# Performance work log

Hardware: AMD Instinct MI355X
Metric: run time of the kernel (lower is better)

The kernel has to match this reference:

```python
import jax, jax.numpy as jnp
import numpy as np

B, C, H, W = 32, 256, 128, 128
VIEWS, K = 9, 3
PAD = (K - 1) // 2


def setup_inputs() -> dict:
    key = jax.random.key(0)
    k1, k2, k3, k4, k5 = jax.random.split(key, 5)
    x = jax.random.normal(k1, (B, C, H, W), dtype=jnp.float32)
    kernels_u = jax.random.normal(k2, (VIEWS, 1, C, K, K), dtype=jnp.float32) * 0.01
    kernels_v = jax.random.normal(k3, (VIEWS, 1, C, K, K), dtype=jnp.float32) * 0.01
    u_indices = jax.random.randint(k4, (B,), 0, VIEWS)
    v_indices = jax.random.randint(k5, (B,), 0, VIEWS)
    return {"x": x, "kernels_u": kernels_u, "kernels_v": kernels_v,
            "u_indices": u_indices, "v_indices": v_indices}


def reference(x, kernels_u, kernels_v, u_indices, v_indices):
    b, c, h, w = x.shape
    # Gather per-sample kernels: [B,1,C,3,3] each
    k_u = kernels_u[u_indices]
    k_v = kernels_v[v_indices]
    # [B,2,C,3,3] -> grouped-conv weights [2B, C, 3, 3]
    weights = jnp.concatenate([k_u, k_v], axis=1).reshape(b * 2, c, K, K)
    # Reflect-pad then treat batch as groups: lhs [1, B*C, H+2p, W+2p]
    x_pad = jnp.pad(x, ((0, 0), (0, 0), (PAD, PAD), (PAD, PAD)), mode="reflect")
    lhs = x_pad.reshape(1, b * c, h + 2 * PAD, w + 2 * PAD)
    out = jax.lax.conv_general_dilated(
        lhs, weights,
        window_strides=(1, 1), padding="VALID",
        dimension_numbers=("NCHW", "OIHW", "NCHW"),
        feature_group_count=b,
    )  # [1, 2B, H, W]
    return out.reshape(b, 2, h, w)
```

## Files before the change

kernel.cpp:

```cpp
#include <hip/hip_runtime.h>

constexpr int Bc = 32;
constexpr int Cc = 256;
constexpr int Hc = 128;
constexpr int Wc = 128;
constexpr int HWc = Hc * Wc;
constexpr int CHUNKS = 4;
constexpr int CPC = Cc / CHUNKS;
constexpr int ROWS = 16;
constexpr int TILES = Hc / ROWS;

__global__ __launch_bounds__(512) void zero_out_kernel(float4* __restrict__ out4) {
    int i = blockIdx.x * 512 + threadIdx.x;
    out4[i] = make_float4(0.f, 0.f, 0.f, 0.f);
}

__global__ __launch_bounds__(512) void modbank_kernel(
    const float* __restrict__ x,
    const float* __restrict__ ku,
    const float* __restrict__ kv,
    const int*   __restrict__ ui,
    const int*   __restrict__ vi,
    float* __restrict__ out)
{
    __shared__ float4 swu[CPC * 3];
    __shared__ float4 swv[CPC * 3];

    const int tile  = blockIdx.x;
    const int b     = blockIdx.y;
    const int chunk = blockIdx.z;
    const int c0    = chunk * CPC;
    const int tid   = threadIdx.x;

    const int uview = ui[b];
    const int vview = vi[b];
    const float* gu = ku + (size_t)uview * (Cc * 9) + c0 * 9;
    const float* gv = kv + (size_t)vview * (Cc * 9) + c0 * 9;
    float* su = (float*)swu;
    float* sv = (float*)swv;
    for (int i = tid; i < CPC * 9; i += 512) {
        int c = i / 9;
        int k = i - c * 9;
        su[c * 12 + k] = gu[i];
        sv[c * 12 + k] = gv[i];
    }
    __syncthreads();

    const int w4 = tid & 31;
    const int r  = tid >> 5;
    const int h  = tile * ROWS + r;
    const int hm = (h == 0)      ? 1      : h - 1;
    const int hp = (h == Hc - 1) ? Hc - 2 : h + 1;

    const float* pm = x + ((size_t)(b * Cc + c0) * Hc + hm) * Wc + w4 * 4;
    const float* p0 = x + ((size_t)(b * Cc + c0) * Hc + h ) * Wc + w4 * 4;
    const float* pp = x + ((size_t)(b * Cc + c0) * Hc + hp) * Wc + w4 * 4;

    float4 au = make_float4(0.f, 0.f, 0.f, 0.f);
    float4 av = make_float4(0.f, 0.f, 0.f, 0.f);

    auto row_acc = [](float l, const float4& v, float rt,
                      float wa, float wb, float wc, float4& acc) {
        acc.x = fmaf(l,   wa, fmaf(v.x, wb, fmaf(v.y, wc, acc.x)));
        acc.y = fmaf(v.x, wa, fmaf(v.y, wb, fmaf(v.z, wc, acc.y)));
        acc.z = fmaf(v.y, wa, fmaf(v.z, wb, fmaf(v.w, wc, acc.z)));
        acc.w = fmaf(v.z, wa, fmaf(v.w, wb, fmaf(rt,  wc, acc.w)));
    };

    for (int ci = 0; ci < CPC; ++ci) {
        const float4 vm = *(const float4*)pm;
        const float4 v0 = *(const float4*)p0;
        const float4 vp = *(const float4*)pp;
        pm += HWc; p0 += HWc; pp += HWc;

        const float4 u0 = swu[ci * 3 + 0];
        const float4 u1 = swu[ci * 3 + 1];
        const float4 u2 = swu[ci * 3 + 2];
        const float4 q0 = swv[ci * 3 + 0];
        const float4 q1 = swv[ci * 3 + 1];
        const float4 q2 = swv[ci * 3 + 2];

        float lm = __shfl_up(vm.w, 1);  float rm = __shfl_down(vm.x, 1);
        float l0 = __shfl_up(v0.w, 1);  float r0 = __shfl_down(v0.x, 1);
        float lp = __shfl_up(vp.w, 1);  float rp = __shfl_down(vp.x, 1);
        if (w4 == 0)  { lm = vm.y; l0 = v0.y; lp = vp.y; }
        if (w4 == 31) { rm = vm.z; r0 = v0.z; rp = vp.z; }

        row_acc(lm, vm, rm, u0.x, u0.y, u0.z, au);
        row_acc(l0, v0, r0, u0.w, u1.x, u1.y, au);
        row_acc(lp, vp, rp, u1.z, u1.w, u2.x, au);
        row_acc(lm, vm, rm, q0.x, q0.y, q0.z, av);
        row_acc(l0, v0, r0, q0.w, q1.x, q1.y, av);
        row_acc(lp, vp, rp, q1.z, q1.w, q2.x, av);
    }

    float* ou = out + ((size_t)(b * 2 + 0) * Hc + h) * Wc + w4 * 4;
    float* ov = out + ((size_t)(b * 2 + 1) * Hc + h) * Wc + w4 * 4;
    atomicAdd(ou + 0, au.x); atomicAdd(ou + 1, au.y);
    atomicAdd(ou + 2, au.z); atomicAdd(ou + 3, au.w);
    atomicAdd(ov + 0, av.x); atomicAdd(ov + 1, av.y);
    atomicAdd(ov + 2, av.z); atomicAdd(ov + 3, av.w);
}

extern "C" void kernel_launch(void* const* d_in, const int* in_sizes, int n_in,
                              void* d_out, int out_size, void* d_ws, size_t ws_size,
                              hipStream_t stream) {
    const float* x  = (const float*)d_in[0];
    const float* ku = (const float*)d_in[1];
    const float* kv = (const float*)d_in[2];
    const int*   ui = (const int*)d_in[3];
    const int*   vi = (const int*)d_in[4];
    float* out = (float*)d_out;

    zero_out_kernel<<<512, 512, 0, stream>>>((float4*)out);

    dim3 grid(TILES, Bc, CHUNKS);
    modbank_kernel<<<grid, 512, 0, stream>>>(x, ku, kv, ui, vi, out);
}
```

Before: 723.4 us.

## Defer horizontal halo exchange to epilogue and read weights directly from global

The per-channel cross-lane shuffles for left/right neighbours are removed. Each lane instead accumulates partial sums for the columns just outside its four-wide segment and exchanges them once after the channel loop, with reflect edges handled by masked multiplies. Weights are now read through uniform global loads instead of being staged in shared memory, which drops the shared-memory fill and the barrier. The channel split goes from 4 chunks to 2, halving the atomic adds, and an occupancy hint plus unroll 2 are added. The trade-off is fewer blocks in the grid and more FMAs per channel.

```diff
diff --git a/kernel.cpp b/kernel.cpp
--- a/kernel.cpp
+++ b/kernel.cpp
@@ -5,7 +5,7 @@
 constexpr int Hc = 128;
 constexpr int Wc = 128;
 constexpr int HWc = Hc * Wc;
-constexpr int CHUNKS = 4;
+constexpr int CHUNKS = 2;
 constexpr int CPC = Cc / CHUNKS;
 constexpr int ROWS = 16;
 constexpr int TILES = Hc / ROWS;
@@ -15,7 +15,7 @@
     out4[i] = make_float4(0.f, 0.f, 0.f, 0.f);
 }
 
-__global__ __launch_bounds__(512) void modbank_kernel(
+__global__ __launch_bounds__(512, 4) void modbank_kernel(
     const float* __restrict__ x,
     const float* __restrict__ ku,
     const float* __restrict__ kv,
@@ -23,28 +23,11 @@
     const int*   __restrict__ vi,
     float* __restrict__ out)
 {
-    __shared__ float4 swu[CPC * 3];
-    __shared__ float4 swv[CPC * 3];
-
     const int tile  = blockIdx.x;
     const int b     = blockIdx.y;
     const int chunk = blockIdx.z;
     const int c0    = chunk * CPC;
     const int tid   = threadIdx.x;
-
-    const int uview = ui[b];
-    const int vview = vi[b];
-    const float* gu = ku + (size_t)uview * (Cc * 9) + c0 * 9;
-    const float* gv = kv + (size_t)vview * (Cc * 9) + c0 * 9;
-    float* su = (float*)swu;
-    float* sv = (float*)swv;
-    for (int i = tid; i < CPC * 9; i += 512) {
-        int c = i / 9;
-        int k = i - c * 9;
-        su[c * 12 + k] = gu[i];
-        sv[c * 12 + k] = gv[i];
-    }
-    __syncthreads();
 
     const int w4 = tid & 31;
     const int r  = tid >> 5;
@@ -56,43 +39,55 @@
     const float* p0 = x + ((size_t)(b * Cc + c0) * Hc + h ) * Wc + w4 * 4;
     const float* pp = x + ((size_t)(b * Cc + c0) * Hc + hp) * Wc + w4 * 4;
 
+    const int uview = ui[b];
+    const int vview = vi[b];
+    const float* wub = ku + ((size_t)uview * Cc + c0) * 9;
+    const float* wvb = kv + ((size_t)vview * Cc + c0) * 9;
+
+    const float eL = (w4 == 0)  ? 1.f : 0.f;
+    const float eR = (w4 == 31) ? 1.f : 0.f;
+
+    float  aum1 = 0.f, au4 = 0.f, avm1 = 0.f, av4 = 0.f;
     float4 au = make_float4(0.f, 0.f, 0.f, 0.f);
     float4 av = make_float4(0.f, 0.f, 0.f, 0.f);
 
-    auto row_acc = [](float l, const float4& v, float rt,
-                      float wa, float wb, float wc, float4& acc) {
-        acc.x = fmaf(l,   wa, fmaf(v.x, wb, fmaf(v.y, wc, acc.x)));
-        acc.y = fmaf(v.x, wa, fmaf(v.y, wb, fmaf(v.z, wc, acc.y)));
-        acc.z = fmaf(v.y, wa, fmaf(v.z, wb, fmaf(v.w, wc, acc.z)));
-        acc.w = fmaf(v.z, wa, fmaf(v.w, wb, fmaf(rt,  wc, acc.w)));
+    auto rowc = [](const float4& v, float tL, float tR,
+                   float ka, float kb, float kc,
+                   float& am1, float4& a, float& a4) {
+        am1 = fmaf(kc, v.x, am1);
+        a.x = fmaf(kb, v.x, fmaf(kc, v.y, fmaf(ka, tL, a.x)));
+        a.y = fmaf(ka, v.x, fmaf(kb, v.y, fmaf(kc, v.z, a.y)));
+        a.z = fmaf(ka, v.y, fmaf(kb, v.z, fmaf(kc, v.w, a.z)));
+        a.w = fmaf(ka, v.z, fmaf(kb, v.w, fmaf(kc, tR, a.w)));
+        a4  = fmaf(ka, v.w, a4);
     };
 
+    #pragma unroll 2
     for (int ci = 0; ci < CPC; ++ci) {
-        const float4 vm = *(const float4*)pm;
-        const float4 v0 = *(const float4*)p0;
-        const float4 vp = *(const float4*)pp;
-        pm += HWc; p0 += HWc; pp += HWc;
+        const float4 vm = *(const float4*)pm; pm += HWc;
+        const float4 v0 = *(const float4*)p0; p0 += HWc;
+        const float4 vp = *(const float4*)pp; pp += HWc;
+        const float* wu = wub + ci * 9;
+        const float* wv = wvb + ci * 9;
 
-        const float4 u0 = swu[ci * 3 + 0];
-        const float4 u1 = swu[ci * 3 + 1];
-        const float4 u2 = swu[ci * 3 + 2];
-        const float4 q0 = swv[ci * 3 + 0];
-        const float4 q1 = swv[ci * 3 + 1];
-        const float4 q2 = swv[ci * 3 + 2];
+        const float tLm = eL * vm.y, tRm = eR * vm.z;
+        const float tL0 = eL * v0.y, tR0 = eR * v0.z;
+        const float tLp = eL * vp.y, tRp = eR * vp.z;
 
-        float lm = __shfl_up(vm.w, 1);  float rm = __shfl_down(vm.x, 1);
-        float l0 = __shfl_up(v0.w, 1);  float r0 = __shfl_down(v0.x, 1);
-        float lp = __shfl_up(vp.w, 1);  float rp = __shfl_down(vp.x, 1);
-        if (w4 == 0)  { lm = vm.y; l0 = v0.y; lp = vp.y; }
-        if (w4 == 31) { rm = vm.z; r0 = v0.z; rp = vp.z; }
+        rowc(vm, tLm, tRm, wu[0], wu[1], wu[2], aum1, au, au4);
+        rowc(v0, tL0, tR0, wu[3], wu[4], wu[5], aum1, au, au4);
+        rowc(vp, tLp, tRp, wu[6], wu[7], wu[8], aum1, au, au4);
+        rowc(vm, tLm, tRm, wv[0], wv[1], wv[2], avm1, av, av4);
+        rowc(v0, tL0, tR0, wv[3], wv[4], wv[5], avm1, av, av4);
+        rowc(vp, tLp, tRp, wv[6], wv[7], wv[8], avm1, av, av4);
+    }
 
-        row_acc(lm, vm, rm, u0.x, u0.y, u0.z, au);
-        row_acc(l0, v0, r0, u0.w, u1.x, u1.y, au);
-        row_acc(lp, vp, rp, u1.z, u1.w, u2.x, au);
-        row_acc(lm, vm, rm, q0.x, q0.y, q0.z, av);
-        row_acc(l0, v0, r0, q0.w, q1.x, q1.y, av);
-        row_acc(lp, vp, rp, q1.z, q1.w, q2.x, av);
-    }
+    float fLu = __shfl_up(au4, 1);    if (w4 == 0)  fLu = 0.f;
+    float fLv = __shfl_up(av4, 1);    if (w4 == 0)  fLv = 0.f;
+    float fRu = __shfl_down(aum1, 1); if (w4 == 31) fRu = 0.f;
+    float fRv = __shfl_down(avm1, 1); if (w4 == 31) fRv = 0.f;
+    au.x += fLu; au.w += fRu;
+    av.x += fLv; av.w += fRv;
 
     float* ou = out + ((size_t)(b * 2 + 0) * Hc + h) * Wc + w4 * 4;
     float* ov = out + ((size_t)(b * 2 + 1) * Hc + h) * Wc + w4 * 4;
```

After: 726.2 us. Within noise of the previous version (+0.4%).
